# Kernel optimization log

Hardware: AMD Instinct MI355X
Metric: run time of the kernel (lower is better)

## Reference

```python
import jax, jax.numpy as jnp
import numpy as np

NA, NS = 50000, 5000          # artist / style node counts
E_AA, E_AS = 500000, 250000   # edges per edge type
C, ED = 128, 8                # hidden dim, edge-attr dim
DIN_A, DIN_S = 128, 64        # input feature dims
NUM_LAYERS = 3


def _l2norm(x):
    # F.normalize(x, dim=-1): x / max(||x||_2, eps)
    n = jnp.sqrt(jnp.sum(x * x, axis=-1, keepdims=True))
    return x / jnp.maximum(n, 1e-12)


def _gatv2(x_src, x_dst, src, dst, eattr, Wl, Wr, att, We, b, num_dst):
    # PyG GATv2Conv, heads=1, concat=True, add_self_loops=False, edge_dim=ED
    xl = x_src @ Wl                      # [Nsrc, C] transformed source
    xr = x_dst @ Wr                      # [Ndst, C] transformed target
    m = xl[src] + xr[dst] + eattr @ We   # [E, C]
    e = jax.nn.leaky_relu(m, 0.2) @ att  # [E] attention logits
    # segment softmax over destination nodes
    emax = jax.ops.segment_max(e, dst, num_segments=num_dst)
    ee = jnp.exp(e - emax[dst])
    den = jax.ops.segment_sum(ee, dst, num_segments=num_dst)
    alpha = ee / jnp.maximum(den[dst], 1e-16)
    out = jax.ops.segment_sum(alpha[:, None] * xl[src], dst, num_segments=num_dst)
    return out + b


def setup_inputs() -> dict:
    key = jax.random.key(0)
    ks = iter(jax.random.split(key, 40))
    r = lambda shape, s=1.0: s * jax.random.normal(next(ks), shape, dtype=jnp.float32)
    d = {}
    d['x_artist'] = r((NA, DIN_A))
    d['x_style'] = r((NS, DIN_S))
    d['src_aa'] = jax.random.randint(next(ks), (E_AA,), 0, NA, dtype=jnp.int32)
    d['dst_aa'] = jax.random.randint(next(ks), (E_AA,), 0, NA, dtype=jnp.int32)
    d['eattr_aa'] = r((E_AA, ED))
    d['src_as'] = jax.random.randint(next(ks), (E_AS,), 0, NA, dtype=jnp.int32)
    d['dst_as'] = jax.random.randint(next(ks), (E_AS,), 0, NS, dtype=jnp.int32)
    d['eattr_as'] = r((E_AS, ED))
    w = 0.1
    # layer 0 (input dims differ per edge type)
    d['Wl0_aa'] = r((DIN_A, C), w); d['Wr0_aa'] = r((DIN_A, C), w)
    d['att0_aa'] = r((C,), w); d['We0_aa'] = r((ED, C), w); d['b0_aa'] = r((C,), w)
    d['Wl0_as'] = r((DIN_A, C), w); d['Wr0_as'] = r((DIN_S, C), w)
    d['att0_as'] = r((C,), w); d['We0_as'] = r((ED, C), w); d['b0_as'] = r((C,), w)
    # layers 1..2 stacked
    d['Wl_aa'] = r((2, C, C), w); d['Wr_aa'] = r((2, C, C), w)
    d['att_aa'] = r((2, C), w); d['We_aa'] = r((2, ED, C), w); d['b_aa'] = r((2, C), w)
    d['Wl_as'] = r((2, C, C), w); d['Wr_as'] = r((2, C, C), w)
    d['att_as'] = r((2, C), w); d['We_as'] = r((2, ED, C), w); d['b_as'] = r((2, C), w)
    return d


def reference(x_artist, x_style, src_aa, dst_aa, eattr_aa, src_as, dst_as, eattr_as,
              Wl0_aa, Wr0_aa, att0_aa, We0_aa, b0_aa,
              Wl0_as, Wr0_as, att0_as, We0_as, b0_as,
              Wl_aa, Wr_aa, att_aa, We_aa, b_aa,
              Wl_as, Wr_as, att_as, We_as, b_as):
    ha, hs = x_artist, x_style
    for i in range(NUM_LAYERS):
        if i == 0:
            p_aa = (Wl0_aa, Wr0_aa, att0_aa, We0_aa, b0_aa)
            p_as = (Wl0_as, Wr0_as, att0_as, We0_as, b0_as)
        else:
            j = i - 1
            p_aa = (Wl_aa[j], Wr_aa[j], att_aa[j], We_aa[j], b_aa[j])
            p_as = (Wl_as[j], Wr_as[j], att_as[j], We_as[j], b_as[j])
        # HeteroConv: each dst node type receives from exactly one edge type here
        na = _gatv2(ha, ha, src_aa, dst_aa, eattr_aa, *p_aa, NA)
        ns = _gatv2(ha, hs, src_as, dst_as, eattr_as, *p_as, NS)
        if i < NUM_LAYERS - 1:
            na = jax.nn.relu(na)
            ns = jax.nn.relu(ns)
        # dropout p=0.0 -> identity; then L2 normalize per node
        ha, hs = _l2norm(na), _l2norm(ns)
    return ha, hs
```

## Files before the change

kernel.cpp:

```cpp
#include <hip/hip_runtime.h>
#include <hip/hip_bf16.h>
#include <math.h>

#define NA 50000
#define NS 5000
#define E_AA 500000
#define E_AS 250000
#define CDIM 128
#define ED 8
#define NAPAD 50176
#define NSPAD 5120
#define SCAN_CH 2048
#define AGG_BLOCKS 1024
#define AGG_BLK_AA 711

typedef __attribute__((ext_vector_type(8))) short bf16x8;
typedef __attribute__((ext_vector_type(4))) float f32x4;

__device__ inline short f2bf(float f) {
    __hip_bfloat16 h = __float2bfloat16(f);
    return *(short*)&h;
}
__device__ inline float bf2f(short s) {
    union { unsigned int u; float f; } cv;
    cv.u = ((unsigned int)(unsigned short)s) << 16;
    return cv.f;
}


__device__ inline float4 f4fma(float s, float4 a, float4 b) {
    return make_float4(fmaf(s, a.x, b.x), fmaf(s, a.y, b.y),
                       fmaf(s, a.z, b.z), fmaf(s, a.w, b.w));
}
__device__ inline float4 f4add(float4 a, float4 b) {
    return make_float4(a.x + b.x, a.y + b.y, a.z + b.z, a.w + b.w);
}
__device__ inline float4 f4leaky(float4 a) {
    return make_float4(a.x > 0.f ? a.x : 0.2f * a.x, a.y > 0.f ? a.y : 0.2f * a.y,
                       a.z > 0.f ? a.z : 0.2f * a.z, a.w > 0.f ? a.w : 0.2f * a.w);
}
__device__ inline float f4dot(float4 a, float4 b) {
    return a.x * b.x + a.y * b.y + a.z * b.z + a.w * b.w;
}
__device__ inline float4 f4mix(float sc, float4 a, float p, float4 x) {
    return make_float4(fmaf(sc, a.x, p * x.x), fmaf(sc, a.y, p * x.y),
                       fmaf(sc, a.z, p * x.z), fmaf(sc, a.w, p * x.w));
}
__device__ inline float4 bfh2f4(bf16x8 v, int half) {
    int o = half * 4;
    return make_float4(bf2f(v[o]), bf2f(v[o + 1]), bf2f(v[o + 2]), bf2f(v[o + 3]));
}


__global__ __launch_bounds__(256) void prep1_k(
    const int* __restrict__ dst0, const int* __restrict__ dst1,
    int* __restrict__ deg0, int* __restrict__ deg1,
    const float* __restrict__ xa, const float* __restrict__ xs,
    short* __restrict__ Xb, short* __restrict__ Xsb,
    const float* __restrict__ Wl0_aa, const float* __restrict__ Wr0_aa,
    const float* __restrict__ Wl0_as, const float* __restrict__ Wr0_as,
    const float* __restrict__ Wl_aa, const float* __restrict__ Wr_aa,
    const float* __restrict__ Wl_as, const float* __restrict__ Wr_as,
    short* __restrict__ Wt, int gCnt, int gCvt) {
    int b = blockIdx.x;
    if (b < gCnt) {
        int e = b * 256 + threadIdx.x;
        if (e < E_AA) atomicAdd(&deg0[dst0[e]], 1);
        if (e < E_AS) atomicAdd(&deg1[dst1[e]], 1);
        return;
    }
    b -= gCnt;
    if (b < gCvt) {
        const int t4A = NAPAD * 32;
        const int t4S = NSPAD * 32;
        int i = b * 256 + threadIdx.x;
        if (i < t4A) {
            int row = i >> 5, c4 = i & 31;
            float4 v = make_float4(0.f, 0.f, 0.f, 0.f);
            if (row < NA) v = ((const float4*)xa)[(size_t)row * 32 + c4];
            short4 s;
            s.x = f2bf(v.x); s.y = f2bf(v.y); s.z = f2bf(v.z); s.w = f2bf(v.w);
            ((short4*)Xb)[i] = s;
        } else if (i < t4A + t4S) {
            int j = i - t4A;
            int row = j >> 5, c4 = j & 31;
            float4 v = make_float4(0.f, 0.f, 0.f, 0.f);
            if (row < NS && c4 < 16) v = ((const float4*)xs)[(size_t)row * 16 + c4];
            short4 s;
            s.x = f2bf(v.x); s.y = f2bf(v.y); s.z = f2bf(v.z); s.w = f2bf(v.w);
            ((short4*)Xsb)[j] = s;
        }
        return;
    }
    b -= gCvt;
    {
        int mat = b >> 6;
        int layer = mat >> 2, w = mat & 3;
        int idx = (b & 63) * 256 + threadIdx.x;
        int k = idx >> 7, n = idx & 127;
        const float* W;
        int K = 128;
        if (layer == 0) {
            W = (w == 0) ? Wl0_aa : (w == 1) ? Wr0_aa : (w == 2) ? Wl0_as : Wr0_as;
            if (w == 3) K = 64;
        } else {
            int j = layer - 1;
            W = ((w == 0) ? Wl_aa : (w == 1) ? Wr_aa : (w == 2) ? Wl_as : Wr_as)
                + (size_t)j * 16384;
        }
        float v = (k < K) ? W[(size_t)k * 128 + n] : 0.f;
        Wt[(size_t)mat * 16384 + n * 128 + k] = f2bf(v);
    }
}

__global__ __launch_bounds__(256) void scanA_k(const int* __restrict__ deg0, int n0,
                                               const int* __restrict__ deg1, int n1,
                                               int nb0, int* __restrict__ bsum) {
    int b = blockIdx.x;
    const int* deg; int n; int lb;
    if ((int)b < nb0) { deg = deg0; n = n0; lb = b; }
    else { deg = deg1; n = n1; lb = b - nb0; }
    int t = threadIdx.x;
    int base = lb * SCAN_CH + t * 8;
    int s = 0;
    #pragma unroll
    for (int i = 0; i < 8; ++i) { int idx = base + i; s += (idx < n) ? deg[idx] : 0; }
    int lane = t & 63, w = t >> 6;
    #pragma unroll
    for (int off = 1; off < 64; off <<= 1) {
        int u = __shfl_up(s, off, 64);
        if (lane >= off) s += u;
    }
    __shared__ int ws[4];
    if (lane == 63) ws[w] = s;
    __syncthreads();
    if (t == 0) bsum[blockIdx.x] = ws[0] + ws[1] + ws[2] + ws[3];
}

__global__ void scanB_k(int* __restrict__ bsum, int nb0, int nb1) {
    int t = threadIdx.x;
    int n = nb0 + nb1;
    int v = (t < n) ? bsum[t] : 0;
    int incl = v;
    #pragma unroll
    for (int off = 1; off < 64; off <<= 1) {
        int u = __shfl_up(incl, off, 64);
        if (t >= off) incl += u;
    }
    int excl = incl - v;
    int sum0 = __shfl(incl, nb0 - 1, 64);
    if (t >= nb0) excl -= sum0;
    if (t < n) bsum[t] = excl;
}

__global__ __launch_bounds__(256) void scanC_k(const int* __restrict__ deg0, int n0,
                                               const int* __restrict__ deg1, int n1,
                                               int nb0, const int* __restrict__ bsum,
                                               int* __restrict__ rs0, int* __restrict__ rs1) {
    int b = blockIdx.x;
    const int* deg; int n; int* rs; int lb;
    if ((int)b < nb0) { deg = deg0; n = n0; rs = rs0; lb = b; }
    else { deg = deg1; n = n1; rs = rs1; lb = b - nb0; }
    int boff = bsum[b];
    int t = threadIdx.x;
    int base = lb * SCAN_CH + t * 8;
    int v[8];
    int tsum = 0;
    #pragma unroll
    for (int i = 0; i < 8; ++i) {
        int idx = base + i;
        v[i] = (idx < n) ? deg[idx] : 0;
        tsum += v[i];
    }
    int lane = t & 63, w = t >> 6;
    int incl = tsum;
    #pragma unroll
    for (int off = 1; off < 64; off <<= 1) {
        int u = __shfl_up(incl, off, 64);
        if (lane >= off) incl += u;
    }
    __shared__ int ws[4];
    if (lane == 63) ws[w] = incl;
    __syncthreads();
    int woff = 0;
    for (int i = 0; i < w; ++i) woff += ws[i];
    int run = boff + woff + incl - tsum;
    #pragma unroll
    for (int i = 0; i < 8; ++i) {
        int idx = base + i;
        if (idx < n) {
            rs[idx] = run;
            run += v[i];
            if (idx == n - 1) rs[n] = run;
        }
    }
}

__global__ __launch_bounds__(256) void scatter2_k(
    const int* __restrict__ dst0, const int* __restrict__ src0, const float* __restrict__ ea0,
    const int* __restrict__ dst1, const int* __restrict__ src1, const float* __restrict__ ea1,
    const int* __restrict__ rs0, const int* __restrict__ rs1,
    int* __restrict__ cur0, int* __restrict__ cur1,
    int* __restrict__ csrsrc0, int* __restrict__ csrsrc1,
    short* __restrict__ eas0, short* __restrict__ eas1) {
    int e = blockIdx.x * 256 + threadIdx.x;
    if (e < E_AA) {
        int d = dst0[e];
        int pos = atomicAdd(&cur0[d], 1);
        int slot = rs0[d] + pos;
        csrsrc0[slot] = src0[e];
        float4 a = ((const float4*)ea0)[(size_t)e * 2];
        float4 b = ((const float4*)ea0)[(size_t)e * 2 + 1];
        bf16x8 pk;
        pk[0] = f2bf(a.x); pk[1] = f2bf(a.y); pk[2] = f2bf(a.z); pk[3] = f2bf(a.w);
        pk[4] = f2bf(b.x); pk[5] = f2bf(b.y); pk[6] = f2bf(b.z); pk[7] = f2bf(b.w);
        *(bf16x8*)(eas0 + (size_t)slot * 8) = pk;
    }
    if (e < E_AS) {
        int d = dst1[e];
        int pos = atomicAdd(&cur1[d], 1);
        int slot = rs1[d] + pos;
        csrsrc1[slot] = src1[e];
        float4 a = ((const float4*)ea1)[(size_t)e * 2];
        float4 b = ((const float4*)ea1)[(size_t)e * 2 + 1];
        bf16x8 pk;
        pk[0] = f2bf(a.x); pk[1] = f2bf(a.y); pk[2] = f2bf(a.z); pk[3] = f2bf(a.w);
        pk[4] = f2bf(b.x); pk[5] = f2bf(b.y); pk[6] = f2bf(b.z); pk[7] = f2bf(b.w);
        *(bf16x8*)(eas1 + (size_t)slot * 8) = pk;
    }
}


__global__ __launch_bounds__(256) void deghist2_k(const int* __restrict__ rs0, int n0,
                                                  const int* __restrict__ rs1, int n1,
                                                  int nb0, int* __restrict__ dh0,
                                                  int* __restrict__ dh1) {
    int b = blockIdx.x;
    const int* rs; int n; int* dh; int lb;
    if ((int)b < nb0) { rs = rs0; n = n0; dh = dh0; lb = b; }
    else { rs = rs1; n = n1; dh = dh1; lb = b - nb0; }
    __shared__ int lh[256];
    int t = threadIdx.x;
    lh[t] = 0;
    __syncthreads();
    int d = lb * 256 + t;
    if (d < n) {
        int deg = rs[d + 1] - rs[d];
        if (deg > 255) deg = 255;
        atomicAdd(&lh[deg], 1);
    }
    __syncthreads();
    if (lh[t]) atomicAdd(&dh[t], lh[t]);
}

__global__ void binscan2_k(const int* __restrict__ dh0, const int* __restrict__ dh1,
                           int* __restrict__ dbo0, int* __restrict__ dbo1) {
    int w = threadIdx.x >> 6, lane = threadIdx.x & 63;
    const int* dh = w ? dh1 : dh0;
    int* dbo = w ? dbo1 : dbo0;
    int v[4]; int s = 0;
    #pragma unroll
    for (int i = 0; i < 4; ++i) { v[i] = dh[lane * 4 + i]; s += v[i]; }
    int incl = s;
    #pragma unroll
    for (int off = 1; off < 64; off <<= 1) {
        int u = __shfl_up(incl, off, 64);
        if (lane >= off) incl += u;
    }
    int run = incl - s;
    #pragma unroll
    for (int i = 0; i < 4; ++i) { dbo[lane * 4 + i] = run; run += v[i]; }
}

__global__ __launch_bounds__(256) void degscatter2_k(const int* __restrict__ rs0, int n0,
                                                     const int* __restrict__ rs1, int n1,
                                                     int nb0,
                                                     const int* __restrict__ dbo0,
                                                     const int* __restrict__ dbo1,
                                                     int* __restrict__ dcur0,
                                                     int* __restrict__ dcur1,
                                                     int4* __restrict__ jobs0,
                                                     int4* __restrict__ jobs1) {
    int b = blockIdx.x;
    const int* rs; int n; const int* dbo; int* dcur; int4* jobs; int lb;
    if ((int)b < nb0) { rs = rs0; n = n0; dbo = dbo0; dcur = dcur0; jobs = jobs0; lb = b; }
    else { rs = rs1; n = n1; dbo = dbo1; dcur = dcur1; jobs = jobs1; lb = b - nb0; }
    __shared__ int lh[256];
    __shared__ int lbase[256];
    int t = threadIdx.x;
    lh[t] = 0;
    __syncthreads();
    int d = lb * 256 + t;
    int deg = 0, lpos = 0, e0 = 0, degc = 0;
    if (d < n) {
        e0 = rs[d];
        deg = rs[d + 1] - e0;
        degc = deg > 255 ? 255 : deg;
        lpos = atomicAdd(&lh[degc], 1);
    }
    __syncthreads();
    int cnt = lh[t];
    if (cnt) lbase[t] = atomicAdd(&dcur[t], cnt);
    __syncthreads();
    if (d < n) jobs[dbo[degc] + lbase[degc] + lpos] = make_int4(d, e0, deg, 0);
}


__global__ __launch_bounds__(256) void gemm4_k(
    const short* __restrict__ Xb, const short* __restrict__ Xsb,
    const short* __restrict__ Wt,
    short* __restrict__ Y0b, short* __restrict__ Y1b, short* __restrict__ Y2b,
    short* __restrict__ Y3b, int gM) {
    int t = threadIdx.x;
    int wave = t >> 6, lane = t & 63;
    int quad = lane >> 4, l16 = lane & 15;
    int gM3 = gM * 3;
    bool style = (int)blockIdx.x >= gM3;
    const short* X = style ? Xsb : Xb;
    int rblk, w;
    if (style) { rblk = (int)blockIdx.x - gM3; w = 3; }
    else { w = (int)blockIdx.x / gM; rblk = (int)blockIdx.x % gM; }
    int rbase = rblk * 256 + wave * 64;

    bf16x8 xf[4][4];
    #pragma unroll
    for (int rt = 0; rt < 4; ++rt) {
        const short* xrow = X + (size_t)(rbase + rt * 16 + l16) * 128 + quad * 8;
        #pragma unroll
        for (int kb = 0; kb < 4; ++kb) xf[rt][kb] = *(const bf16x8*)(xrow + kb * 32);
    }

    short* Y = style ? Y3b : (w == 0 ? Y0b : (w == 1 ? Y1b : Y2b));
    int nlim = style ? NS : NA;
    const short* Wb = Wt + (size_t)w * 16384;
    #pragma unroll 2
    for (int nt = 0; nt < 8; ++nt) {
        const short* wrow = Wb + (size_t)(nt * 16 + l16) * 128 + quad * 8;
        bf16x8 wf[4];
        #pragma unroll
        for (int kb = 0; kb < 4; ++kb) wf[kb] = *(const bf16x8*)(wrow + kb * 32);
        f32x4 acc[4] = {{0,0,0,0},{0,0,0,0},{0,0,0,0},{0,0,0,0}};
        #pragma unroll
        for (int kb = 0; kb < 4; ++kb)
            #pragma unroll
            for (int rt = 0; rt < 4; ++rt)
                acc[rt] = __builtin_amdgcn_mfma_f32_16x16x32_bf16(wf[kb], xf[rt][kb],
                                                                  acc[rt], 0, 0, 0);
        #pragma unroll
        for (int rt = 0; rt < 4; ++rt) {
            int node = rbase + rt * 16 + l16;
            if (node < nlim) {
                short4 s;
                s.x = f2bf(acc[rt][0]); s.y = f2bf(acc[rt][1]);
                s.z = f2bf(acc[rt][2]); s.w = f2bf(acc[rt][3]);
                *(short4*)(Y + (size_t)node * 128 + nt * 16 + quad * 4) = s;
            }
        }
    }
}


template<bool RELU>
__global__ __launch_bounds__(256, 2) void agg2_k(
    const short* __restrict__ xl0, const short* __restrict__ xr0,
    const short* __restrict__ eas0, const int* __restrict__ csrsrc0,
    const float* __restrict__ We0, const float* __restrict__ att0,
    const float* __restrict__ bias0, const int4* __restrict__ jobs0,
    float* __restrict__ out0, short* __restrict__ outb0, int nd0, int nblk0,
    const short* __restrict__ xl1, const short* __restrict__ xr1,
    const short* __restrict__ eas1, const int* __restrict__ csrsrc1,
    const float* __restrict__ We1, const float* __restrict__ att1,
    const float* __restrict__ bias1, const int4* __restrict__ jobs1,
    float* __restrict__ out1, short* __restrict__ outb1, int nd1, int nblk1,
    int nblkB0) {

    int wave = threadIdx.x >> 6;
    int lane = threadIdx.x & 63;
    int g = lane >> 4;
    int sl = lane & 15;
    int c = sl * 8;

    const short* xl; const short* xrp; const short* eas; const int* csrsrc;
    const float* We; const float* att; const float* bias;
    const int4* jobs;
    float* out; short* outb; int ndst, nblk, blk, stride;
    if ((int)blockIdx.x < nblkB0) {
        xl = xl0; xrp = xr0; eas = eas0; csrsrc = csrsrc0; We = We0; att = att0; bias = bias0;
        jobs = jobs0; out = out0; outb = outb0; ndst = nd0; nblk = nblk0;
        blk = blockIdx.x; stride = nblkB0;
    } else {
        xl = xl1; xrp = xr1; eas = eas1; csrsrc = csrsrc1; We = We1; att = att1; bias = bias1;
        jobs = jobs1; out = out1; outb = outb1; ndst = nd1; nblk = nblk1;
        blk = blockIdx.x - nblkB0; stride = gridDim.x - nblkB0;
    }
    if (blk >= nblk) return;

    float4 WeA[8], WeB[8];
    #pragma unroll
    for (int k = 0; k < 8; ++k) {
        WeA[k] = *(const float4*)(We + k * 128 + c);
        WeB[k] = *(const float4*)(We + k * 128 + c + 4);
    }
    float4 attA = *(const float4*)(att + c);
    float4 attB = *(const float4*)(att + c + 4);
    float4 bA = *(const float4*)(bias + c);
    float4 bB = *(const float4*)(bias + c + 4);
    #pragma unroll
    for (int k = 0; k < 8; ++k) {
        asm volatile("" : "+v"(WeA[k].x), "+v"(WeA[k].y), "+v"(WeA[k].z), "+v"(WeA[k].w));
        asm volatile("" : "+v"(WeB[k].x), "+v"(WeB[k].y), "+v"(WeB[k].z), "+v"(WeB[k].w));
    }
    asm volatile("" : "+v"(attA.x), "+v"(attA.y), "+v"(attA.z), "+v"(attA.w));
    asm volatile("" : "+v"(attB.x), "+v"(attB.y), "+v"(attB.z), "+v"(attB.w));

    auto load_job = [&](int b) -> int4 {
        int di = b * 16 + wave * 4 + g;
        bool h = di < ndst;
        int4 j = jobs[h ? (ndst - 1 - di) : 0];
        if (!h) j.z = 0;
        j.w = h ? 1 : 0;
        return j;
    };

    int4 jb = load_job(blk);
    bf16x8 xrb = *(const bf16x8*)(xrp + (size_t)jb.x * 128 + c);

    for (; blk < nblk; blk += stride) {
        int nb = blk + stride;
        int4 jbN = (nb < nblk) ? load_job(nb) : make_int4(0, 0, 0, 0);

        int d = jb.x, e0 = jb.y, cnt = jb.z;
        bool has = jb.w != 0;
        float4 xrA = bfh2f4(xrb, 0), xrB = bfh2f4(xrb, 1);

        float4 accA = {0,0,0,0}, accB = {0,0,0,0};
        float den = 0.f, mrun = -INFINITY;
        int last = (cnt > 0) ? e0 + cnt - 1 : 0;

        int mc = cnt;
        mc = max(mc, __shfl_xor(mc, 16, 64));
        mc = max(mc, __shfl_xor(mc, 32, 64));
        int niter = (mc + 3) >> 2;

        auto lds_idx = [&](int ib, int* s) {
            #pragma unroll
            for (int j = 0; j < 4; ++j) {
                int cj = (ib + j < last) ? ib + j : last;
                s[j] = csrsrc[cj];
            }
        };
        auto lds_ea = [&](int ib, bf16x8* ea) {
            #pragma unroll
            for (int j = 0; j < 4; ++j) {
                int cj = (ib + j < last) ? ib + j : last;
                ea[j] = *(const bf16x8*)(eas + (size_t)cj * 8);
            }
        };
        auto lds_x = [&](const int* s, bf16x8* xb) {
            #pragma unroll
            for (int j = 0; j < 4; ++j)
                xb[j] = *(const bf16x8*)(xl + (size_t)s[j] * 128 + c);
        };

        int sA[4], sB[4];
        bf16x8 xbA[4], xbB[4], eaA[4], eaB[4];

        if (niter > 0) {
            int st[4];
            lds_idx(e0, st);
            lds_ea(e0, eaA);
            lds_x(st, xbA);
            lds_idx(e0 + 4, sA);
        }

        auto step = [&](int i, bf16x8 (&xbC)[4], bf16x8 (&eaC)[4], int (&sNx)[4],
                        bf16x8 (&xbN)[4], bf16x8 (&eaN)[4], int (&sN2)[4]) {
            lds_x(sNx, xbN);
            lds_ea(e0 + i + 4, eaN);
            lds_idx(e0 + i + 8, sN2);

            float4 x0A = bfh2f4(xbC[0], 0), x0B = bfh2f4(xbC[0], 1);
            float4 x1A = bfh2f4(xbC[1], 0), x1B = bfh2f4(xbC[1], 1);
            float4 x2A = bfh2f4(xbC[2], 0), x2B = bfh2f4(xbC[2], 1);
            float4 x3A = bfh2f4(xbC[3], 0), x3B = bfh2f4(xbC[3], 1);

            auto logit = [&](float4 xA, float4 xB, bf16x8 eab) -> float {
                float4 ea = bfh2f4(eab, 0), eb = bfh2f4(eab, 1);
                float4 mA = f4add(xA, xrA), mB = f4add(xB, xrB);
                mA = f4fma(ea.x, WeA[0], mA); mB = f4fma(ea.x, WeB[0], mB);
                mA = f4fma(ea.y, WeA[1], mA); mB = f4fma(ea.y, WeB[1], mB);
                mA = f4fma(ea.z, WeA[2], mA); mB = f4fma(ea.z, WeB[2], mB);
                mA = f4fma(ea.w, WeA[3], mA); mB = f4fma(ea.w, WeB[3], mB);
                mA = f4fma(eb.x, WeA[4], mA); mB = f4fma(eb.x, WeB[4], mB);
                mA = f4fma(eb.y, WeA[5], mA); mB = f4fma(eb.y, WeB[5], mB);
                mA = f4fma(eb.z, WeA[6], mA); mB = f4fma(eb.z, WeB[6], mB);
                mA = f4fma(eb.w, WeA[7], mA); mB = f4fma(eb.w, WeB[7], mB);
                return f4dot(f4leaky(mA), attA) + f4dot(f4leaky(mB), attB);
            };

            float t0 = logit(x0A, x0B, eaC[0]);
            float t1 = logit(x1A, x1B, eaC[1]);
            float t2 = logit(x2A, x2B, eaC[2]);
            float t3 = logit(x3A, x3B, eaC[3]);
            #pragma unroll
            for (int off = 8; off; off >>= 1) {
                t0 += __shfl_xor(t0, off, 64);
                t1 += __shfl_xor(t1, off, 64);
                t2 += __shfl_xor(t2, off, 64);
                t3 += __shfl_xor(t3, off, 64);
            }
            if (i + 1 >= cnt) t1 = -INFINITY;
            if (i + 2 >= cnt) t2 = -INFINITY;
            if (i + 3 >= cnt) t3 = -INFINITY;

            if (i < cnt) {
                float m4 = fmaxf(fmaxf(t0, t1), fmaxf(t2, t3));
                float nm = fmaxf(mrun, m4);
                float sc = __expf(mrun - nm);
                float p0 = __expf(t0 - nm);
                float p1 = __expf(t1 - nm);
                float p2 = __expf(t2 - nm);
                float p3 = __expf(t3 - nm);
                den = den * sc + p0 + p1 + p2 + p3;
                accA = f4mix(sc, accA, p0, x0A);
                accA = f4fma(p1, x1A, accA);
                accA = f4fma(p2, x2A, accA);
                accA = f4fma(p3, x3A, accA);
                accB = f4mix(sc, accB, p0, x0B);
                accB = f4fma(p1, x1B, accB);
                accB = f4fma(p2, x2B, accB);
                accB = f4fma(p3, x3B, accB);
                mrun = nm;
            }
        };

        int it = 0;
        for (; it + 1 < niter; it += 2) {
            step(it * 4,     xbA, eaA, sA, xbB, eaB, sB);
            step(it * 4 + 4, xbB, eaB, sB, xbA, eaA, sA);
        }
        if (it < niter)
            step(it * 4, xbA, eaA, sA, xbB, eaB, sB);

        float inv = 1.f / fmaxf(den, 1e-16f);
        float4 oA = make_float4(accA.x * inv + bA.x, accA.y * inv + bA.y,
                                accA.z * inv + bA.z, accA.w * inv + bA.w);
        float4 oB = make_float4(accB.x * inv + bB.x, accB.y * inv + bB.y,
                                accB.z * inv + bB.z, accB.w * inv + bB.w);
        if (RELU) {
            oA = make_float4(fmaxf(oA.x,0.f), fmaxf(oA.y,0.f),
                             fmaxf(oA.z,0.f), fmaxf(oA.w,0.f));
            oB = make_float4(fmaxf(oB.x,0.f), fmaxf(oB.y,0.f),
                             fmaxf(oB.z,0.f), fmaxf(oB.w,0.f));
        }
        float ss = f4dot(oA, oA) + f4dot(oB, oB);
        #pragma unroll
        for (int off = 8; off; off >>= 1) ss += __shfl_xor(ss, off, 64);
        float innv = 1.f / fmaxf(sqrtf(ss), 1e-12f);
        oA = make_float4(oA.x * innv, oA.y * innv, oA.z * innv, oA.w * innv);
        oB = make_float4(oB.x * innv, oB.y * innv, oB.z * innv, oB.w * innv);
        if (has) {
            if (out) {
                float4* op = (float4*)(out + (size_t)d * 128 + c);
                op[0] = oA;
                op[1] = oB;
            }
            if (outb) {
                bf16x8 pk;
                pk[0] = f2bf(oA.x); pk[1] = f2bf(oA.y); pk[2] = f2bf(oA.z); pk[3] = f2bf(oA.w);
                pk[4] = f2bf(oB.x); pk[5] = f2bf(oB.y); pk[6] = f2bf(oB.z); pk[7] = f2bf(oB.w);
                *(bf16x8*)(outb + (size_t)d * 128 + c) = pk;
            }
        }

        bf16x8 xrbN = *(const bf16x8*)(xrp + (size_t)jbN.x * 128 + c);
        jb = jbN;
        xrb = xrbN;
    }
}


extern "C" void kernel_launch(void* const* d_in, const int* in_sizes, int n_in,
                              void* d_out, int out_size, void* d_ws, size_t ws_size,
                              hipStream_t stream) {
    const float* x_artist = (const float*)d_in[0];
    const float* x_style  = (const float*)d_in[1];
    const int*   src_aa   = (const int*)d_in[2];
    const int*   dst_aa   = (const int*)d_in[3];
    const float* eattr_aa = (const float*)d_in[4];
    const int*   src_as   = (const int*)d_in[5];
    const int*   dst_as   = (const int*)d_in[6];
    const float* eattr_as = (const float*)d_in[7];
    const float* Wl0_aa = (const float*)d_in[8];
    const float* Wr0_aa = (const float*)d_in[9];
    const float* att0_aa = (const float*)d_in[10];
    const float* We0_aa = (const float*)d_in[11];
    const float* b0_aa = (const float*)d_in[12];
    const float* Wl0_as = (const float*)d_in[13];
    const float* Wr0_as = (const float*)d_in[14];
    const float* att0_as = (const float*)d_in[15];
    const float* We0_as = (const float*)d_in[16];
    const float* b0_as = (const float*)d_in[17];
    const float* Wl_aa = (const float*)d_in[18];
    const float* Wr_aa = (const float*)d_in[19];
    const float* att_aa = (const float*)d_in[20];
    const float* We_aa = (const float*)d_in[21];
    const float* b_aa = (const float*)d_in[22];
    const float* Wl_as = (const float*)d_in[23];
    const float* Wr_as = (const float*)d_in[24];
    const float* att_as = (const float*)d_in[25];
    const float* We_as = (const float*)d_in[26];
    const float* b_as = (const float*)d_in[27];

    float* out = (float*)d_out;

    short* Xb    = (short*)d_ws;
    short* Xsb   = Xb + (size_t)NAPAD * 128;
    short* Wt    = Xsb + (size_t)NSPAD * 128;
    short* bufAb = Wt + 12 * 16384;
    short* bufDb = bufAb + (size_t)NA * 128;
    short* bufBb = bufDb + (size_t)NA * 128;
    short* bufCb = bufBb + (size_t)NA * 128;
    short* easAA = bufCb + (size_t)NSPAD * 128;
    short* easAS = easAA + (size_t)E_AA * 8;
    int* ip = (int*)(easAS + (size_t)E_AS * 8);
    int* zbase  = ip;
    int* deg_aa = ip;            ip += NA;
    int* cur_aa = ip;            ip += NA;
    int* deg_as = ip;            ip += NS;
    int* cur_as = ip;            ip += NS;
    int* dh_aa  = ip;            ip += 256;
    int* dh_as  = ip;            ip += 256;
    int* dcur_aa = ip;           ip += 256;
    int* dcur_as = ip;           ip += 256;
    size_t zbytes = (size_t)(ip - zbase) * sizeof(int);
    int4* jobs_aa = (int4*)ip;   ip += 4 * NA;
    int4* jobs_as = (int4*)ip;   ip += 4 * NS;
    int* rs_aa  = ip;            ip += NA + 1;
    int* rs_as  = ip;            ip += NS + 1;
    int* csrsrc_aa = ip;         ip += E_AA;
    int* csrsrc_as = ip;         ip += E_AS;
    int* dbo_aa = ip;            ip += 256;
    int* dbo_as = ip;            ip += 256;
    int* bsum   = ip;            ip += 64;

    const int nbA_scan = (NA + SCAN_CH - 1) / SCAN_CH;
    const int nbS_scan = (NS + SCAN_CH - 1) / SCAN_CH;
    const int nbA_node = (NA + 255) / 256;
    const int nbS_node = (NS + 255) / 256;
    const int gE = (E_AA + 255) / 256;
    const int gCvt = (NAPAD * 32 + NSPAD * 32 + 255) / 256;
    const int gWtr = 12 * 64;

    hipMemsetAsync(zbase, 0, zbytes, stream);
    prep1_k<<<gE + gCvt + gWtr, 256, 0, stream>>>(
        dst_aa, dst_as, deg_aa, deg_as,
        x_artist, x_style, Xb, Xsb,
        Wl0_aa, Wr0_aa, Wl0_as, Wr0_as, Wl_aa, Wr_aa, Wl_as, Wr_as, Wt,
        gE, gCvt);
    scanA_k<<<nbA_scan + nbS_scan, 256, 0, stream>>>(deg_aa, NA, deg_as, NS, nbA_scan, bsum);
    scanB_k<<<1, 64, 0, stream>>>(bsum, nbA_scan, nbS_scan);
    scanC_k<<<nbA_scan + nbS_scan, 256, 0, stream>>>(deg_aa, NA, deg_as, NS, nbA_scan,
                                                     bsum, rs_aa, rs_as);
    scatter2_k<<<gE, 256, 0, stream>>>(dst_aa, src_aa, eattr_aa,
                                       dst_as, src_as, eattr_as,
                                       rs_aa, rs_as, cur_aa, cur_as,
                                       csrsrc_aa, csrsrc_as, easAA, easAS);
    deghist2_k<<<nbA_node + nbS_node, 256, 0, stream>>>(rs_aa, NA, rs_as, NS, nbA_node,
                                                        dh_aa, dh_as);
    binscan2_k<<<1, 128, 0, stream>>>(dh_aa, dh_as, dbo_aa, dbo_as);
    degscatter2_k<<<nbA_node + nbS_node, 256, 0, stream>>>(rs_aa, NA, rs_as, NS, nbA_node,
                                                           dbo_aa, dbo_as, dcur_aa, dcur_as,
                                                           jobs_aa, jobs_as);

    const int gM = NAPAD / 256;
    const int gS4 = NSPAD / 256;
    const int aggA = (NA + 15) / 16;
    const int aggS = (NS + 15) / 16;

    for (int layer = 0; layer < 3; ++layer) {
        int j = layer - 1;
        const float *patt_aa, *pWe_aa, *pb_aa, *patt_as, *pWe_as, *pb_as;
        if (layer == 0) {
            patt_aa = att0_aa; pWe_aa = We0_aa; pb_aa = b0_aa;
            patt_as = att0_as; pWe_as = We0_as; pb_as = b0_as;
        } else {
            patt_aa = att_aa + (size_t)j * CDIM;
            pWe_aa = We_aa + (size_t)j * ED * CDIM;
            pb_aa = b_aa + (size_t)j * CDIM;
            patt_as = att_as + (size_t)j * CDIM;
            pWe_as = We_as + (size_t)j * ED * CDIM;
            pb_as = b_as + (size_t)j * CDIM;
        }
        const short* pWt = Wt + (size_t)layer * 4 * 16384;
        float* hA_out = (layer == 2) ? out : nullptr;
        float* hS_out = (layer == 2) ? out + (size_t)NA * CDIM : nullptr;
        short* hA_outb = (layer == 2) ? nullptr : Xb;
        short* hS_outb = (layer == 2) ? nullptr : Xsb;

        gemm4_k<<<3 * gM + gS4, 256, 0, stream>>>(Xb, Xsb, pWt, bufAb, bufBb, bufDb, bufCb, gM);

        if (layer < 2)
            agg2_k<true><<<AGG_BLOCKS, 256, 0, stream>>>(
                bufAb, bufBb, easAA, csrsrc_aa, pWe_aa, patt_aa, pb_aa,
                jobs_aa, hA_out, hA_outb, NA, aggA,
                bufDb, bufCb, easAS, csrsrc_as, pWe_as, patt_as, pb_as,
                jobs_as, hS_out, hS_outb, NS, aggS, AGG_BLK_AA);
        else
            agg2_k<false><<<AGG_BLOCKS, 256, 0, stream>>>(
                bufAb, bufBb, easAA, csrsrc_aa, pWe_aa, patt_aa, pb_aa,
                jobs_aa, hA_out, hA_outb, NA, aggA,
                bufDb, bufCb, easAS, csrsrc_as, pWe_as, patt_as, pb_as,
                jobs_as, hS_out, hS_outb, NS, aggS, AGG_BLK_AA);
    }
}
```

Before: 505.3 us.

## Merge scan/binscan kernels via last-block pattern and add atomic work stealing in aggregation

The single-block scanB and binscan kernels are folded into their preceding kernels: the last block to finish, detected with an atomic done counter and thread fences, performs the small scan. This removes two kernel launches. The aggregation kernel now takes its work items from per-edge-type atomic counters instead of a static grid stride, which should balance degree-sorted jobs across blocks. In exchange it adds two extra __syncthreads and an atomic per job, and needs zeroed counters for each layer.

```diff
diff --git a/kernel.cpp b/kernel.cpp
--- a/kernel.cpp
+++ b/kernel.cpp
@@ -113,9 +113,11 @@
     }
 }
 
-__global__ __launch_bounds__(256) void scanA_k(const int* __restrict__ deg0, int n0,
-                                               const int* __restrict__ deg1, int n1,
-                                               int nb0, int* __restrict__ bsum) {
+__global__ __launch_bounds__(256) void scanAB_k(const int* __restrict__ deg0, int n0,
+                                                const int* __restrict__ deg1, int n1,
+                                                int nb0, int nb1,
+                                                int* __restrict__ bsum,
+                                                int* __restrict__ done) {
     int b = blockIdx.x;
     const int* deg; int n; int lb;
     if ((int)b < nb0) { deg = deg0; n = n0; lb = b; }
@@ -135,22 +137,26 @@
     if (lane == 63) ws[w] = s;
     __syncthreads();
     if (t == 0) bsum[blockIdx.x] = ws[0] + ws[1] + ws[2] + ws[3];
-}
-
-__global__ void scanB_k(int* __restrict__ bsum, int nb0, int nb1) {
-    int t = threadIdx.x;
-    int n = nb0 + nb1;
-    int v = (t < n) ? bsum[t] : 0;
-    int incl = v;
-    #pragma unroll
-    for (int off = 1; off < 64; off <<= 1) {
-        int u = __shfl_up(incl, off, 64);
-        if (t >= off) incl += u;
-    }
-    int excl = incl - v;
-    int sum0 = __shfl(incl, nb0 - 1, 64);
-    if (t >= nb0) excl -= sum0;
-    if (t < n) bsum[t] = excl;
+
+    __threadfence();
+    __shared__ int lastFlag;
+    if (t == 0) lastFlag = (atomicAdd(done, 1) == nb0 + nb1 - 1) ? 1 : 0;
+    __syncthreads();
+    if (lastFlag && t < 64) {
+        __threadfence();
+        int nb = nb0 + nb1;
+        int v = (t < nb) ? bsum[t] : 0;
+        int incl = v;
+        #pragma unroll
+        for (int off = 1; off < 64; off <<= 1) {
+            int u = __shfl_up(incl, off, 64);
+            if (t >= off) incl += u;
+        }
+        int excl = incl - v;
+        int sum0 = __shfl(incl, nb0 - 1, 64);
+        if (t >= nb0) excl -= sum0;
+        if (t < nb) bsum[t] = excl;
+    }
 }
 
 __global__ __launch_bounds__(256) void scanC_k(const int* __restrict__ deg0, int n0,
@@ -231,10 +237,13 @@
 }
 
 
-__global__ __launch_bounds__(256) void deghist2_k(const int* __restrict__ rs0, int n0,
-                                                  const int* __restrict__ rs1, int n1,
-                                                  int nb0, int* __restrict__ dh0,
-                                                  int* __restrict__ dh1) {
+__global__ __launch_bounds__(256) void deghist2b_k(const int* __restrict__ rs0, int n0,
+                                                   const int* __restrict__ rs1, int n1,
+                                                   int nb0, int* __restrict__ dh0,
+                                                   int* __restrict__ dh1,
+                                                   int* __restrict__ dbo0,
+                                                   int* __restrict__ dbo1,
+                                                   int* __restrict__ done) {
     int b = blockIdx.x;
     const int* rs; int n; int* dh; int lb;
     if ((int)b < nb0) { rs = rs0; n = n0; dh = dh0; lb = b; }
@@ -251,25 +260,29 @@
     }
     __syncthreads();
     if (lh[t]) atomicAdd(&dh[t], lh[t]);
-}
-
-__global__ void binscan2_k(const int* __restrict__ dh0, const int* __restrict__ dh1,
-                           int* __restrict__ dbo0, int* __restrict__ dbo1) {
-    int w = threadIdx.x >> 6, lane = threadIdx.x & 63;
-    const int* dh = w ? dh1 : dh0;
-    int* dbo = w ? dbo1 : dbo0;
-    int v[4]; int s = 0;
-    #pragma unroll
-    for (int i = 0; i < 4; ++i) { v[i] = dh[lane * 4 + i]; s += v[i]; }
-    int incl = s;
-    #pragma unroll
-    for (int off = 1; off < 64; off <<= 1) {
-        int u = __shfl_up(incl, off, 64);
-        if (lane >= off) incl += u;
-    }
-    int run = incl - s;
-    #pragma unroll
-    for (int i = 0; i < 4; ++i) { dbo[lane * 4 + i] = run; run += v[i]; }
+
+    __threadfence();
+    __shared__ int lastFlag;
+    if (t == 0) lastFlag = (atomicAdd(done, 1) == (int)gridDim.x - 1) ? 1 : 0;
+    __syncthreads();
+    if (lastFlag && t < 128) {
+        __threadfence();
+        int w = t >> 6, lane = t & 63;
+        const int* dhp = w ? dh1 : dh0;
+        int* dbo = w ? dbo1 : dbo0;
+        int v[4]; int s = 0;
+        #pragma unroll
+        for (int i = 0; i < 4; ++i) { v[i] = dhp[lane * 4 + i]; s += v[i]; }
+        int incl = s;
+        #pragma unroll
+        for (int off = 1; off < 64; off <<= 1) {
+            int u = __shfl_up(incl, off, 64);
+            if (lane >= off) incl += u;
+        }
+        int run = incl - s;
+        #pragma unroll
+        for (int i = 0; i < 4; ++i) { dbo[lane * 4 + i] = run; run += v[i]; }
+    }
 }
 
 __global__ __launch_bounds__(256) void degscatter2_k(const int* __restrict__ rs0, int n0,
@@ -372,7 +385,7 @@
     const float* __restrict__ We1, const float* __restrict__ att1,
     const float* __restrict__ bias1, const int4* __restrict__ jobs1,
     float* __restrict__ out1, short* __restrict__ outb1, int nd1, int nblk1,
-    int nblkB0) {
+    int nblkB0, int* __restrict__ ctrs) {
 
     int wave = threadIdx.x >> 6;
     int lane = threadIdx.x & 63;
@@ -383,16 +396,26 @@
     const short* xl; const short* xrp; const short* eas; const int* csrsrc;
     const float* We; const float* att; const float* bias;
     const int4* jobs;
-    float* out; short* outb; int ndst, nblk, blk, stride;
+    float* out; short* outb; int ndst, nblk; int* ctr;
     if ((int)blockIdx.x < nblkB0) {
         xl = xl0; xrp = xr0; eas = eas0; csrsrc = csrsrc0; We = We0; att = att0; bias = bias0;
         jobs = jobs0; out = out0; outb = outb0; ndst = nd0; nblk = nblk0;
-        blk = blockIdx.x; stride = nblkB0;
+        ctr = ctrs;
     } else {
         xl = xl1; xrp = xr1; eas = eas1; csrsrc = csrsrc1; We = We1; att = att1; bias = bias1;
         jobs = jobs1; out = out1; outb = outb1; ndst = nd1; nblk = nblk1;
-        blk = blockIdx.x - nblkB0; stride = gridDim.x - nblkB0;
-    }
+        ctr = ctrs + 1;
+    }
+
+    __shared__ int sjob;
+    auto steal = [&]() -> int {
+        __syncthreads();
+        if (threadIdx.x == 0) sjob = atomicAdd(ctr, 1);
+        __syncthreads();
+        return sjob;
+    };
+
+    int blk = steal();
     if (blk >= nblk) return;
 
     float4 WeA[8], WeB[8];
@@ -425,8 +448,8 @@
     int4 jb = load_job(blk);
     bf16x8 xrb = *(const bf16x8*)(xrp + (size_t)jb.x * 128 + c);
 
-    for (; blk < nblk; blk += stride) {
-        int nb = blk + stride;
+    for (;;) {
+        int nb = steal();
         int4 jbN = (nb < nblk) ? load_job(nb) : make_int4(0, 0, 0, 0);
 
         int d = jb.x, e0 = jb.y, cnt = jb.z;
@@ -573,9 +596,9 @@
             }
         }
 
-        bf16x8 xrbN = *(const bf16x8*)(xrp + (size_t)jbN.x * 128 + c);
+        if (nb >= nblk) break;
+        xrb = *(const bf16x8*)(xrp + (size_t)jbN.x * 128 + c);
         jb = jbN;
-        xrb = xrbN;
     }
 }
 
@@ -633,6 +656,9 @@
     int* dh_as  = ip;            ip += 256;
     int* dcur_aa = ip;           ip += 256;
     int* dcur_as = ip;           ip += 256;
+    int* aggctr = ip;            ip += 8;
+    int* sdone  = ip;            ip += 4;
+    int* hdone  = ip;            ip += 4;
     size_t zbytes = (size_t)(ip - zbase) * sizeof(int);
     int4* jobs_aa = (int4*)ip;   ip += 4 * NA;
     int4* jobs_as = (int4*)ip;   ip += 4 * NS;
@@ -658,17 +684,17 @@
         x_artist, x_style, Xb, Xsb,
         Wl0_aa, Wr0_aa, Wl0_as, Wr0_as, Wl_aa, Wr_aa, Wl_as, Wr_as, Wt,
         gE, gCvt);
-    scanA_k<<<nbA_scan + nbS_scan, 256, 0, stream>>>(deg_aa, NA, deg_as, NS, nbA_scan, bsum);
-    scanB_k<<<1, 64, 0, stream>>>(bsum, nbA_scan, nbS_scan);
+    scanAB_k<<<nbA_scan + nbS_scan, 256, 0, stream>>>(deg_aa, NA, deg_as, NS,
+                                                      nbA_scan, nbS_scan, bsum, sdone);
     scanC_k<<<nbA_scan + nbS_scan, 256, 0, stream>>>(deg_aa, NA, deg_as, NS, nbA_scan,
                                                      bsum, rs_aa, rs_as);
     scatter2_k<<<gE, 256, 0, stream>>>(dst_aa, src_aa, eattr_aa,
                                        dst_as, src_as, eattr_as,
                                        rs_aa, rs_as, cur_aa, cur_as,
                                        csrsrc_aa, csrsrc_as, easAA, easAS);
-    deghist2_k<<<nbA_node + nbS_node, 256, 0, stream>>>(rs_aa, NA, rs_as, NS, nbA_node,
-                                                        dh_aa, dh_as);
-    binscan2_k<<<1, 128, 0, stream>>>(dh_aa, dh_as, dbo_aa, dbo_as);
+    deghist2b_k<<<nbA_node + nbS_node, 256, 0, stream>>>(rs_aa, NA, rs_as, NS, nbA_node,
+                                                         dh_aa, dh_as, dbo_aa, dbo_as,
+                                                         hdone);
     degscatter2_k<<<nbA_node + nbS_node, 256, 0, stream>>>(rs_aa, NA, rs_as, NS, nbA_node,
                                                            dbo_aa, dbo_as, dcur_aa, dcur_as,
                                                            jobs_aa, jobs_as);
@@ -705,12 +731,14 @@
                 bufAb, bufBb, easAA, csrsrc_aa, pWe_aa, patt_aa, pb_aa,
                 jobs_aa, hA_out, hA_outb, NA, aggA,
                 bufDb, bufCb, easAS, csrsrc_as, pWe_as, patt_as, pb_as,
-                jobs_as, hS_out, hS_outb, NS, aggS, AGG_BLK_AA);
+                jobs_as, hS_out, hS_outb, NS, aggS, AGG_BLK_AA,
+                aggctr + 2 * layer);
         else
             agg2_k<false><<<AGG_BLOCKS, 256, 0, stream>>>(
                 bufAb, bufBb, easAA, csrsrc_aa, pWe_aa, patt_aa, pb_aa,
                 jobs_aa, hA_out, hA_outb, NA, aggA,
                 bufDb, bufCb, easAS, csrsrc_as, pWe_as, patt_as, pb_as,
-                jobs_as, hS_out, hS_outb, NS, aggS, AGG_BLK_AA);
-    }
-}
+                jobs_as, hS_out, hS_outb, NS, aggS, AGG_BLK_AA,
+                aggctr + 2 * layer);
+    }
+}
```

Result: slower. 658.5 us (+30.3%).

## Fuse scan and degree-sort kernel chains using last-block grid synchronization

Applied to the files above, without the earlier changes.

Merges the three-kernel block scan (scanA/scanB/scanC) into one kernel and the histogram/binscan/degscatter chain into one kernel. In each, the last block to finish (found through an atomic counter) does the small serial scan, then releases a flag that all blocks spin on. This removes four kernel launches and their gaps in preprocessing. It relies on every block being resident at once for the spin-wait to be safe, which holds for these small grids (about 27 and 216 blocks), and it moves the dcur atomics to a point before the bin offsets are known.

```diff
diff --git a/kernel.cpp b/kernel.cpp
--- a/kernel.cpp
+++ b/kernel.cpp
@@ -113,55 +113,19 @@
     }
 }
 
-__global__ __launch_bounds__(256) void scanA_k(const int* __restrict__ deg0, int n0,
-                                               const int* __restrict__ deg1, int n1,
-                                               int nb0, int* __restrict__ bsum) {
-    int b = blockIdx.x;
-    const int* deg; int n; int lb;
-    if ((int)b < nb0) { deg = deg0; n = n0; lb = b; }
-    else { deg = deg1; n = n1; lb = b - nb0; }
-    int t = threadIdx.x;
-    int base = lb * SCAN_CH + t * 8;
-    int s = 0;
-    #pragma unroll
-    for (int i = 0; i < 8; ++i) { int idx = base + i; s += (idx < n) ? deg[idx] : 0; }
-    int lane = t & 63, w = t >> 6;
-    #pragma unroll
-    for (int off = 1; off < 64; off <<= 1) {
-        int u = __shfl_up(s, off, 64);
-        if (lane >= off) s += u;
-    }
-    __shared__ int ws[4];
-    if (lane == 63) ws[w] = s;
-    __syncthreads();
-    if (t == 0) bsum[blockIdx.x] = ws[0] + ws[1] + ws[2] + ws[3];
-}
-
-__global__ void scanB_k(int* __restrict__ bsum, int nb0, int nb1) {
-    int t = threadIdx.x;
-    int n = nb0 + nb1;
-    int v = (t < n) ? bsum[t] : 0;
-    int incl = v;
-    #pragma unroll
-    for (int off = 1; off < 64; off <<= 1) {
-        int u = __shfl_up(incl, off, 64);
-        if (t >= off) incl += u;
-    }
-    int excl = incl - v;
-    int sum0 = __shfl(incl, nb0 - 1, 64);
-    if (t >= nb0) excl -= sum0;
-    if (t < n) bsum[t] = excl;
-}
-
-__global__ __launch_bounds__(256) void scanC_k(const int* __restrict__ deg0, int n0,
-                                               const int* __restrict__ deg1, int n1,
-                                               int nb0, const int* __restrict__ bsum,
-                                               int* __restrict__ rs0, int* __restrict__ rs1) {
+
+__global__ __launch_bounds__(256) void scanABC_k(const int* __restrict__ deg0, int n0,
+                                                 const int* __restrict__ deg1, int n1,
+                                                 int nb0, int nb1,
+                                                 int* __restrict__ bsum,
+                                                 int* __restrict__ done,
+                                                 int* __restrict__ flag,
+                                                 int* __restrict__ rs0,
+                                                 int* __restrict__ rs1) {
     int b = blockIdx.x;
     const int* deg; int n; int* rs; int lb;
     if ((int)b < nb0) { deg = deg0; n = n0; rs = rs0; lb = b; }
     else { deg = deg1; n = n1; rs = rs1; lb = b - nb0; }
-    int boff = bsum[b];
     int t = threadIdx.x;
     int base = lb * SCAN_CH + t * 8;
     int v[8];
@@ -182,6 +146,46 @@
     __shared__ int ws[4];
     if (lane == 63) ws[w] = incl;
     __syncthreads();
+    if (t == 0) {
+        int bs = ws[0] + ws[1] + ws[2] + ws[3];
+        __hip_atomic_store(&bsum[blockIdx.x], bs, __ATOMIC_RELEASE,
+                           __HIP_MEMORY_SCOPE_AGENT);
+    }
+
+    __shared__ int lastFlag;
+    if (t == 0) lastFlag = (atomicAdd(done, 1) == nb0 + nb1 - 1) ? 1 : 0;
+    __syncthreads();
+    if (lastFlag) {
+        if (t < 64) {
+            int nb = nb0 + nb1;
+            int vv = (t < nb) ? __hip_atomic_load(&bsum[t], __ATOMIC_ACQUIRE,
+                                                  __HIP_MEMORY_SCOPE_AGENT) : 0;
+            int inc2 = vv;
+            #pragma unroll
+            for (int off = 1; off < 64; off <<= 1) {
+                int u = __shfl_up(inc2, off, 64);
+                if (t >= off) inc2 += u;
+            }
+            int excl = inc2 - vv;
+            int sum0 = __shfl(inc2, nb0 - 1, 64);
+            if (t >= nb0) excl -= sum0;
+            if (t < nb)
+                __hip_atomic_store(&bsum[t], excl, __ATOMIC_RELEASE,
+                                   __HIP_MEMORY_SCOPE_AGENT);
+        }
+        __syncthreads();
+        if (t == 0)
+            __hip_atomic_store(flag, 1, __ATOMIC_RELEASE, __HIP_MEMORY_SCOPE_AGENT);
+    }
+
+    if (t == 0) {
+        while (__hip_atomic_load(flag, __ATOMIC_ACQUIRE, __HIP_MEMORY_SCOPE_AGENT) == 0)
+            __builtin_amdgcn_s_sleep(8);
+    }
+    __syncthreads();
+
+    int boff = __hip_atomic_load(&bsum[blockIdx.x], __ATOMIC_ACQUIRE,
+                                 __HIP_MEMORY_SCOPE_AGENT);
     int woff = 0;
     for (int i = 0; i < w; ++i) woff += ws[i];
     int run = boff + woff + incl - tsum;
@@ -231,60 +235,18 @@
 }
 
 
-__global__ __launch_bounds__(256) void deghist2_k(const int* __restrict__ rs0, int n0,
-                                                  const int* __restrict__ rs1, int n1,
-                                                  int nb0, int* __restrict__ dh0,
-                                                  int* __restrict__ dh1) {
+__global__ __launch_bounds__(256) void degsort_k(const int* __restrict__ rs0, int n0,
+                                                 const int* __restrict__ rs1, int n1,
+                                                 int nb0,
+                                                 int* __restrict__ dh0, int* __restrict__ dh1,
+                                                 int* __restrict__ dbo0, int* __restrict__ dbo1,
+                                                 int* __restrict__ dcur0, int* __restrict__ dcur1,
+                                                 int4* __restrict__ jobs0, int4* __restrict__ jobs1,
+                                                 int* __restrict__ done, int* __restrict__ flag) {
     int b = blockIdx.x;
-    const int* rs; int n; int* dh; int lb;
-    if ((int)b < nb0) { rs = rs0; n = n0; dh = dh0; lb = b; }
-    else { rs = rs1; n = n1; dh = dh1; lb = b - nb0; }
-    __shared__ int lh[256];
-    int t = threadIdx.x;
-    lh[t] = 0;
-    __syncthreads();
-    int d = lb * 256 + t;
-    if (d < n) {
-        int deg = rs[d + 1] - rs[d];
-        if (deg > 255) deg = 255;
-        atomicAdd(&lh[deg], 1);
-    }
-    __syncthreads();
-    if (lh[t]) atomicAdd(&dh[t], lh[t]);
-}
-
-__global__ void binscan2_k(const int* __restrict__ dh0, const int* __restrict__ dh1,
-                           int* __restrict__ dbo0, int* __restrict__ dbo1) {
-    int w = threadIdx.x >> 6, lane = threadIdx.x & 63;
-    const int* dh = w ? dh1 : dh0;
-    int* dbo = w ? dbo1 : dbo0;
-    int v[4]; int s = 0;
-    #pragma unroll
-    for (int i = 0; i < 4; ++i) { v[i] = dh[lane * 4 + i]; s += v[i]; }
-    int incl = s;
-    #pragma unroll
-    for (int off = 1; off < 64; off <<= 1) {
-        int u = __shfl_up(incl, off, 64);
-        if (lane >= off) incl += u;
-    }
-    int run = incl - s;
-    #pragma unroll
-    for (int i = 0; i < 4; ++i) { dbo[lane * 4 + i] = run; run += v[i]; }
-}
-
-__global__ __launch_bounds__(256) void degscatter2_k(const int* __restrict__ rs0, int n0,
-                                                     const int* __restrict__ rs1, int n1,
-                                                     int nb0,
-                                                     const int* __restrict__ dbo0,
-                                                     const int* __restrict__ dbo1,
-                                                     int* __restrict__ dcur0,
-                                                     int* __restrict__ dcur1,
-                                                     int4* __restrict__ jobs0,
-                                                     int4* __restrict__ jobs1) {
-    int b = blockIdx.x;
-    const int* rs; int n; const int* dbo; int* dcur; int4* jobs; int lb;
-    if ((int)b < nb0) { rs = rs0; n = n0; dbo = dbo0; dcur = dcur0; jobs = jobs0; lb = b; }
-    else { rs = rs1; n = n1; dbo = dbo1; dcur = dcur1; jobs = jobs1; lb = b - nb0; }
+    const int* rs; int n; int* dh; int* dbo; int* dcur; int4* jobs; int lb;
+    if ((int)b < nb0) { rs = rs0; n = n0; dh = dh0; dbo = dbo0; dcur = dcur0; jobs = jobs0; lb = b; }
+    else { rs = rs1; n = n1; dh = dh1; dbo = dbo1; dcur = dcur1; jobs = jobs1; lb = b - nb0; }
     __shared__ int lh[256];
     __shared__ int lbase[256];
     int t = threadIdx.x;
@@ -300,9 +262,57 @@
     }
     __syncthreads();
     int cnt = lh[t];
-    if (cnt) lbase[t] = atomicAdd(&dcur[t], cnt);
+    if (cnt) {
+        atomicAdd(&dh[t], cnt);
+        lbase[t] = atomicAdd(&dcur[t], cnt);
+    }
     __syncthreads();
-    if (d < n) jobs[dbo[degc] + lbase[degc] + lpos] = make_int4(d, e0, deg, 0);
+
+    __shared__ int lastFlag;
+    if (t == 0) lastFlag = (atomicAdd(done, 1) == (int)gridDim.x - 1) ? 1 : 0;
+    __syncthreads();
+    if (lastFlag) {
+        if (t < 128) {
+            int w2 = t >> 6, lane = t & 63;
+            int* dhp = w2 ? dh1 : dh0;
+            int* dbop = w2 ? dbo1 : dbo0;
+            int vv[4]; int s = 0;
+            #pragma unroll
+            for (int i = 0; i < 4; ++i) {
+                vv[i] = __hip_atomic_load(&dhp[lane * 4 + i], __ATOMIC_ACQUIRE,
+                                          __HIP_MEMORY_SCOPE_AGENT);
+                s += vv[i];
+            }
+            int incl = s;
+            #pragma unroll
+            for (int off = 1; off < 64; off <<= 1) {
+                int u = __shfl_up(incl, off, 64);
+                if (lane >= off) incl += u;
+            }
+            int run = incl - s;
+            #pragma unroll
+            for (int i = 0; i < 4; ++i) {
+                __hip_atomic_store(&dbop[lane * 4 + i], run, __ATOMIC_RELEASE,
+                                   __HIP_MEMORY_SCOPE_AGENT);
+                run += vv[i];
+            }
+        }
+        __syncthreads();
+        if (t == 0)
+            __hip_atomic_store(flag, 1, __ATOMIC_RELEASE, __HIP_MEMORY_SCOPE_AGENT);
+    }
+
+    if (t == 0) {
+        while (__hip_atomic_load(flag, __ATOMIC_ACQUIRE, __HIP_MEMORY_SCOPE_AGENT) == 0)
+            __builtin_amdgcn_s_sleep(8);
+    }
+    __syncthreads();
+
+    if (d < n) {
+        int binb = __hip_atomic_load(&dbo[degc], __ATOMIC_ACQUIRE,
+                                     __HIP_MEMORY_SCOPE_AGENT);
+        jobs[binb + lbase[degc] + lpos] = make_int4(d, e0, deg, 0);
+    }
 }
 
 
@@ -633,6 +643,8 @@
     int* dh_as  = ip;            ip += 256;
     int* dcur_aa = ip;           ip += 256;
     int* dcur_as = ip;           ip += 256;
+    int* sdone  = ip;            ip += 2;
+    int* hdone  = ip;            ip += 2;
     size_t zbytes = (size_t)(ip - zbase) * sizeof(int);
     int4* jobs_aa = (int4*)ip;   ip += 4 * NA;
     int4* jobs_as = (int4*)ip;   ip += 4 * NS;
@@ -658,20 +670,19 @@
         x_artist, x_style, Xb, Xsb,
         Wl0_aa, Wr0_aa, Wl0_as, Wr0_as, Wl_aa, Wr_aa, Wl_as, Wr_as, Wt,
         gE, gCvt);
-    scanA_k<<<nbA_scan + nbS_scan, 256, 0, stream>>>(deg_aa, NA, deg_as, NS, nbA_scan, bsum);
-    scanB_k<<<1, 64, 0, stream>>>(bsum, nbA_scan, nbS_scan);
-    scanC_k<<<nbA_scan + nbS_scan, 256, 0, stream>>>(deg_aa, NA, deg_as, NS, nbA_scan,
-                                                     bsum, rs_aa, rs_as);
+    scanABC_k<<<nbA_scan + nbS_scan, 256, 0, stream>>>(deg_aa, NA, deg_as, NS,
+                                                       nbA_scan, nbS_scan, bsum,
+                                                       sdone, sdone + 1,
+                                                       rs_aa, rs_as);
     scatter2_k<<<gE, 256, 0, stream>>>(dst_aa, src_aa, eattr_aa,
                                        dst_as, src_as, eattr_as,
                                        rs_aa, rs_as, cur_aa, cur_as,
                                        csrsrc_aa, csrsrc_as, easAA, easAS);
-    deghist2_k<<<nbA_node + nbS_node, 256, 0, stream>>>(rs_aa, NA, rs_as, NS, nbA_node,
-                                                        dh_aa, dh_as);
-    binscan2_k<<<1, 128, 0, stream>>>(dh_aa, dh_as, dbo_aa, dbo_as);
-    degscatter2_k<<<nbA_node + nbS_node, 256, 0, stream>>>(rs_aa, NA, rs_as, NS, nbA_node,
-                                                           dbo_aa, dbo_as, dcur_aa, dcur_as,
-                                                           jobs_aa, jobs_as);
+    degsort_k<<<nbA_node + nbS_node, 256, 0, stream>>>(rs_aa, NA, rs_as, NS, nbA_node,
+                                                       dh_aa, dh_as, dbo_aa, dbo_as,
+                                                       dcur_aa, dcur_as,
+                                                       jobs_aa, jobs_as,
+                                                       hdone, hdone + 1);
 
     const int gM = NAPAD / 256;
     const int gS4 = NSPAD / 256;
```

New measurement: 528.2 us. 1.05x slower.
